# Optimization experiments

Measured on AMD Instinct MI355X. Metric: run time of the kernel, lower is better.

The kernel has to match this reference:

```python
import jax, jax.numpy as jnp
import numpy as np
import math

B, S, H = 2, 2048, 2048
NH, HD = 16, 128
THETA = 10000.0
NEG = -1e9


def make_rope_tables(seq_len, head_dim, theta):
    inv_freq = 1.0 / (theta ** (np.arange(0, head_dim, 2, dtype=np.float32) / head_dim))
    pos = np.arange(seq_len, dtype=np.float32)
    freqs = np.outer(pos, inv_freq)                    # (S, HD/2)
    emb = np.concatenate([freqs, freqs], axis=-1)      # (S, HD)
    return jnp.asarray(np.cos(emb)), jnp.asarray(np.sin(emb))


def setup_inputs() -> dict:
    key = jax.random.key(0)
    k1, k2, k3 = jax.random.split(key, 3)
    hidden_states = jax.random.normal(k1, (B, S, H), dtype=jnp.float32)
    rope_cos, rope_sin = make_rope_tables(S, HD, THETA)
    # additive causal mask [1,1,S,S]
    causal = jnp.tril(jnp.ones((S, S), dtype=bool))
    attention_mask = jnp.where(causal, 0.0, NEG).astype(jnp.float32)[None, None]
    w_qkv = jax.random.normal(k2, (3 * H, H), dtype=jnp.float32) * (1.0 / math.sqrt(H))
    w_o = jax.random.normal(k3, (H, H), dtype=jnp.float32) * (1.0 / math.sqrt(H))
    return {"hidden_states": hidden_states, "rope_cos": rope_cos, "rope_sin": rope_sin,
            "attention_mask": attention_mask, "w_qkv": w_qkv, "w_o": w_o}


def apply_rope(x, cos, sin):
    # x: (B, NH, S, HD); cos/sin: (S, HD)
    half = x.shape[-1] // 2
    x1, x2 = x[..., :half], x[..., half:]
    x_rot = jnp.concatenate([-x2, x1], axis=-1)
    return x * cos[None, None] + x_rot * sin[None, None]


def reference(hidden_states, rope_cos, rope_sin, attention_mask, w_qkv, w_o):
    b, s, h = hidden_states.shape
    qkv = hidden_states @ w_qkv.T                      # (B, S, 3H)
    qkv = qkv.reshape(b, s, 3, NH, HD).transpose(2, 0, 3, 1, 4)  # (3, B, NH, S, HD)
    q, k, v = qkv[0], qkv[1], qkv[2]
    q = apply_rope(q, rope_cos, rope_sin)
    k = apply_rope(k, rope_cos, rope_sin)
    scale = 1.0 / math.sqrt(HD)
    scores = jnp.einsum('bhqd,bhkd->bhqk', q, k) * scale + attention_mask
    probs = jax.nn.softmax(scores.astype(jnp.float32), axis=-1).astype(q.dtype)
    out = jnp.einsum('bhqk,bhkd->bhqd', probs, v)      # (B, NH, S, HD)
    out = out.transpose(0, 2, 1, 3).reshape(b, s, h)
    return out @ w_o.T
```

## Files before the change

### kernel.cpp

```cpp
#include <hip/hip_runtime.h>
#include <stdint.h>

typedef unsigned int u32;
typedef unsigned short u16;

typedef __bf16 bf16x8 __attribute__((ext_vector_type(8)));
typedef float f32x4 __attribute__((ext_vector_type(4)));

struct alignas(16) V16 { u32 a, b, c, d; };

__device__ __forceinline__ u16 f2bf(float x) {
    u32 u = __float_as_uint(x);
    u += 0x7FFFu + ((u >> 16) & 1u);
    return (u16)(u >> 16);
}
__device__ __forceinline__ float bf2f(u16 h) {
    return __uint_as_float(((u32)h) << 16);
}

__device__ __forceinline__ bf16x8 ld_frag(const u16* p) {
    return __builtin_bit_cast(bf16x8, *(const V16*)p);
}

__device__ __forceinline__ void async_cp16(u16* lds_dst, const u16* g_src) {
    __builtin_amdgcn_global_load_lds(
        (__attribute__((address_space(1))) void*)g_src,
        (__attribute__((address_space(3))) void*)lds_dst, 16, 0, 0);
}

__global__ __launch_bounds__(256) void cast_all_kernel(
    const float* __restrict__ hidden, const float* __restrict__ wqkv,
    const float* __restrict__ wo,
    u16* __restrict__ hA, u16* __restrict__ wqb, u16* __restrict__ wob)
{
    int i = blockIdx.x * 256 + threadIdx.x;
    const float* src; u16* dst; int off;
    if (i < 2097152)      { src = hidden; dst = hA;  off = i; }
    else if (i < 5242880) { src = wqkv;   dst = wqb; off = i - 2097152; }
    else                  { src = wo;     dst = wob; off = i - 5242880; }
    const float* p = src + (size_t)off * 4;
    ushort4 o;
    o.x = f2bf(p[0]); o.y = f2bf(p[1]); o.z = f2bf(p[2]); o.w = f2bf(p[3]);
    *(ushort4*)(dst + (size_t)off * 4) = o;
}

__device__ __forceinline__ void stage_half(
    u16* smem, const u16* __restrict__ Ag, const u16* __restrict__ Bg,
    int K, int isB, int kk, int buf, int th, int w, int rg0, int chl)
{
    const u16* G = isB ? Bg : Ag;
    u16* base = smem + isB * 32768 + buf * 16384 + kk * 8192;
    const int kcol = th * 64 + kk * 32;
#pragma unroll
    for (int i = 0; i < 2; ++i) {
        const int s = i * 8 + w;
        const int rg = s * 16 + rg0;
        async_cp16(base + s * 512, G + (size_t)rg * K + kcol + chl * 8);
    }
}

__global__ __launch_bounds__(512, 2) void gemm256(
    const u16* __restrict__ A, const u16* __restrict__ Bt,
    int M, int N, int K, int mode,
    float* __restrict__ Cout,
    u16* __restrict__ Qb, u16* __restrict__ Kb, u16* __restrict__ Vtb)
{
    extern __shared__ u16 smem[];
    const int t = threadIdx.x;
    const int w = t >> 6, l = t & 63;
    const int lr = l & 15, lk = (l >> 4) * 8;
    const int wm16 = (w >> 2) * 8;
    const int wn16 = (w & 3) * 4;
    const int laneoff = lr * 32 + (lk ^ ((lr & 8) ? 16 : 0));
    const int rg0 = l >> 2;
    const int chl = (l & 3) ^ ((l >> 4) & 2);

    const int flat = blockIdx.y * gridDim.x + blockIdx.x;
    const int xcd = flat & 7, slot = flat >> 3;
    const int cpx = gridDim.x >> 3;
    const int ncol = xcd * cpx + slot % cpx;
    const int mrow = slot / cpx;
    const int m0 = mrow * 256, n0 = ncol * 256;

    const u16* Ag = A + (size_t)m0 * K;
    const u16* Bg = Bt + (size_t)n0 * K;

    f32x4 acc[8][4];
#pragma unroll
    for (int i = 0; i < 8; ++i)
#pragma unroll
        for (int j = 0; j < 4; ++j) acc[i][j] = f32x4{0.f, 0.f, 0.f, 0.f};

    const int NT = K >> 6;

    stage_half(smem, Ag, Bg, K, 0, 0, 0, 0, w, rg0, chl);
    stage_half(smem, Ag, Bg, K, 1, 0, 0, 0, w, rg0, chl);
    stage_half(smem, Ag, Bg, K, 0, 1, 0, 0, w, rg0, chl);
    stage_half(smem, Ag, Bg, K, 1, 1, 0, 0, w, rg0, chl);
    stage_half(smem, Ag, Bg, K, 0, 0, 1, 1, w, rg0, chl);
    stage_half(smem, Ag, Bg, K, 1, 0, 1, 1, w, rg0, chl);
    asm volatile("s_waitcnt vmcnt(8)" ::: "memory");
    __builtin_amdgcn_s_barrier();

    for (int tt = 0; tt < NT; tt += 2) {
#pragma unroll
        for (int sub = 0; sub < 2; ++sub) {
            const int tcur = tt + sub;
            const u16* Abuf = smem + sub * 16384;
            const u16* Bbuf = smem + 32768 + sub * 16384;
            bf16x8 bfr[4];
#pragma unroll
            for (int p = 0; p < 4; ++p) {
                const int kk = p >> 1, mh = p & 1;
                const u16* Ab = Abuf + kk * 8192;
                const u16* Bb = Bbuf + kk * 8192;
                if (mh == 0) {
#pragma unroll
                    for (int ni = 0; ni < 4; ++ni)
                        bfr[ni] = ld_frag(Bb + (wn16 + ni) * 512 + laneoff);
                }
                bf16x8 af[4];
#pragma unroll
                for (int i = 0; i < 4; ++i)
                    af[i] = ld_frag(Ab + (wm16 + mh * 4 + i) * 512 + laneoff);

                if (p == 0 && tcur + 1 < NT)
                    stage_half(smem, Ag, Bg, K, 0, 1, sub ^ 1, tcur + 1, w, rg0, chl);
                if (p == 1 && tcur + 1 < NT)
                    stage_half(smem, Ag, Bg, K, 1, 1, sub ^ 1, tcur + 1, w, rg0, chl);
                if (p == 2 && tcur + 2 < NT)
                    stage_half(smem, Ag, Bg, K, 0, 0, sub, tcur + 2, w, rg0, chl);
                if (p == 3 && tcur + 2 < NT)
                    stage_half(smem, Ag, Bg, K, 1, 0, sub, tcur + 2, w, rg0, chl);

                if (p == 1) {
                    if (tcur < NT - 1) asm volatile("s_waitcnt vmcnt(8)" ::: "memory");
                    else               asm volatile("s_waitcnt vmcnt(0)" ::: "memory");
                }
                if (p == 3) {
                    if (tcur < NT - 2)       asm volatile("s_waitcnt vmcnt(8)" ::: "memory");
                    else if (tcur == NT - 2) asm volatile("s_waitcnt vmcnt(4)" ::: "memory");
                }
                __builtin_amdgcn_s_barrier();
                __builtin_amdgcn_s_setprio(1);
#pragma unroll
                for (int i = 0; i < 4; ++i)
#pragma unroll
                    for (int ni = 0; ni < 4; ++ni)
                        acc[mh * 4 + i][ni] = __builtin_amdgcn_mfma_f32_16x16x32_bf16(
                            af[i], bfr[ni], acc[mh * 4 + i][ni], 0, 0, 0);
                __builtin_amdgcn_s_setprio(0);
                __builtin_amdgcn_s_barrier();
            }
        }
    }

    __syncthreads();
    const int lrow4 = (l >> 4) * 4;
    const int wm0 = (w >> 2) * 128, wn0 = (w & 3) * 64;

    if (mode == 1) {
#pragma unroll
        for (int mi = 0; mi < 8; ++mi)
#pragma unroll
            for (int ni = 0; ni < 4; ++ni)
#pragma unroll
                for (int r = 0; r < 4; ++r) {
                    int gr = m0 + wm0 + mi * 16 + lrow4 + r;
                    int gc = n0 + wn0 + ni * 16 + lr;
                    Cout[(size_t)gr * N + gc] = acc[mi][ni][r];
                }
        return;
    }

    const int which = n0 >> 11;
    const int nh0 = (n0 & 2047) >> 7;
    const int bb = m0 >> 11;
    const int s0 = m0 & 2047;

    if (which < 2) {
#pragma unroll
        for (int mi = 0; mi < 8; ++mi)
#pragma unroll
            for (int ni = 0; ni < 4; ++ni)
#pragma unroll
                for (int r = 0; r < 4; ++r)
                    smem[(wm0 + mi * 16 + lrow4 + r) * 256 + wn0 + ni * 16 + lr] =
                        f2bf(acc[mi][ni][r]);
    } else {
#pragma unroll
        for (int mi = 0; mi < 8; ++mi)
#pragma unroll
            for (int ni = 0; ni < 4; ++ni)
#pragma unroll
                for (int r = 0; r < 4; ++r) {
                    int cr = wn0 + ni * 16 + lr;
                    int cc = wm0 + mi * 16 + lrow4 + r;
                    smem[cr * 256 + (cc ^ ((cr & 7) << 3))] = f2bf(acc[mi][ni][r]);
                }
    }
    __syncthreads();

    if (which < 2) {
        u16* dstb = (which == 0 ? Qb : Kb);
#pragma unroll
        for (int ps = 0; ps < 16; ++ps) {
            int chunk = ps * 512 + t;
            int row = chunk >> 5;
            int ce = (chunk & 31) * 8;
            int head = nh0 + (ce >> 7);
            int d = ce & 127;
            *(V16*)&dstb[((size_t)(bb * 16 + head) * 2048 + s0 + row) * 128 + d] =
                *(const V16*)&smem[row * 256 + ce];
        }
    } else {
#pragma unroll
        for (int ps = 0; ps < 16; ++ps) {
            int chunk = ps * 512 + t;
            int drow = chunk >> 5;
            int se = (chunk & 31) * 8;
            int head = nh0 + (drow >> 7);
            int d = drow & 127;
            *(V16*)&Vtb[((size_t)(bb * 16 + head) * 128 + d) * 2048 + s0 + se] =
                *(const V16*)&smem[drow * 256 + (se ^ ((drow & 7) << 3))];
        }
    }
}

__global__ __launch_bounds__(256) void gemm_bt(
    const u16* __restrict__ A, const u16* __restrict__ Bt,
    int M, int N, int K, int mode,
    float* __restrict__ Cout,
    u16* __restrict__ Qb, u16* __restrict__ Kb, u16* __restrict__ Vtb)
{
    __shared__ u16 smem[17408];
    u16* As = smem;
    u16* Bs = smem + 8192;

    const int t = threadIdx.x;
    const int w = t >> 6, l = t & 63;
    const int lr = l & 15;
    const int lk = (l >> 4) * 8;

    const int flat = blockIdx.y * gridDim.x + blockIdx.x;
    const int xcd = flat & 7, slot = flat >> 3;
    const int cpx = gridDim.x >> 3;
    const int ncol = xcd * cpx + slot % cpx;
    const int mrow = slot / cpx;
    const int m0 = mrow * 128, n0 = ncol * 128;
    const int wm = (w >> 1) * 64, wn = (w & 1) * 64;

    f32x4 acc[4][4];
#pragma unroll
    for (int i = 0; i < 4; ++i)
#pragma unroll
        for (int j = 0; j < 4; ++j) acc[i][j] = f32x4{0.f, 0.f, 0.f, 0.f};

    const u16* Ag = A + (size_t)m0 * K;
    const u16* Bg = Bt + (size_t)n0 * K;
    const int srow = l >> 2;
    const int scol = (l & 3) * 8;

    for (int k0 = 0; k0 < K; k0 += 64) {
#pragma unroll
        for (int g = 0; g < 2; ++g) {
            const int row = w * 32 + g * 16;
#pragma unroll
            for (int c = 0; c < 2; ++c) {
                async_cp16(&As[c * 4096 + row * 32],
                           Ag + (size_t)(row + srow) * K + k0 + c * 32 + scol);
                async_cp16(&Bs[c * 4096 + row * 32],
                           Bg + (size_t)(row + srow) * K + k0 + c * 32 + scol);
            }
        }
        __syncthreads();

#pragma unroll
        for (int c = 0; c < 2; ++c) {
            bf16x8 af[4], bf[4];
#pragma unroll
            for (int i = 0; i < 4; ++i)
                af[i] = ld_frag(&As[c * 4096 + (wm + i * 16 + lr) * 32 + lk]);
#pragma unroll
            for (int j = 0; j < 4; ++j)
                bf[j] = ld_frag(&Bs[c * 4096 + (wn + j * 16 + lr) * 32 + lk]);
#pragma unroll
            for (int i = 0; i < 4; ++i)
#pragma unroll
                for (int j = 0; j < 4; ++j)
                    acc[i][j] = __builtin_amdgcn_mfma_f32_16x16x32_bf16(af[i], bf[j], acc[i][j], 0, 0, 0);
        }
        __syncthreads();
    }

    const int lrow4 = (l >> 4) * 4;
    if (mode == 1) {
#pragma unroll
        for (int i = 0; i < 4; ++i)
#pragma unroll
            for (int j = 0; j < 4; ++j)
#pragma unroll
                for (int r = 0; r < 4; ++r) {
                    int gr = m0 + wm + i * 16 + lrow4 + r;
                    int gc = n0 + wn + j * 16 + lr;
                    Cout[(size_t)gr * N + gc] = acc[i][j][r];
                }
    } else {
        const int which = n0 >> 11;
        const int nh = (n0 & 2047) >> 7;
        const int bb = m0 >> 11;
        const int s0 = m0 & 2047;
        u16* Cs = smem;
        if (which < 2) {
#pragma unroll
            for (int i = 0; i < 4; ++i)
#pragma unroll
                for (int j = 0; j < 4; ++j)
#pragma unroll
                    for (int r = 0; r < 4; ++r)
                        Cs[(wm + i * 16 + lrow4 + r) * 136 + wn + j * 16 + lr] =
                            f2bf(acc[i][j][r]);
        } else {
#pragma unroll
            for (int i = 0; i < 4; ++i)
#pragma unroll
                for (int j = 0; j < 4; ++j)
#pragma unroll
                    for (int r = 0; r < 4; ++r)
                        Cs[(wn + j * 16 + lr) * 136 + wm + i * 16 + lrow4 + r] =
                            f2bf(acc[i][j][r]);
        }
        __syncthreads();
        const int rrow = t >> 4, rcol = (t & 15) * 8;
        if (which < 2) {
            u16* dst = (which == 0 ? Qb : Kb) +
                       ((size_t)(bb * 16 + nh) * 2048 + s0) * 128;
#pragma unroll
            for (int it = 0; it < 8; ++it) {
                int row = it * 16 + rrow;
                *(V16*)&dst[(size_t)row * 128 + rcol] = *(const V16*)&Cs[row * 136 + rcol];
            }
        } else {
            u16* dst = Vtb + (size_t)(bb * 16 + nh) * 128 * 2048 + s0;
#pragma unroll
            for (int it = 0; it < 8; ++it) {
                int d = it * 16 + rrow;
                *(V16*)&dst[(size_t)d * 2048 + rcol] = *(const V16*)&Cs[d * 136 + rcol];
            }
        }
    }
}

__global__ __launch_bounds__(256) void rope_kernel(
    u16* __restrict__ Qb, u16* __restrict__ Kb,
    const float* __restrict__ cosT, const float* __restrict__ sinT, float qscale)
{
    int idx = blockIdx.x * 256 + threadIdx.x;
    int d = (idx & 7) * 8;
    int s = (idx >> 3) & 2047;
    int bh = idx >> 14;
    size_t base = ((size_t)bh * 2048 + s) * 128;
    float c[8], sn[8];
#pragma unroll
    for (int i = 0; i < 8; ++i) {
        c[i]  = cosT[s * 128 + d + i];
        sn[i] = sinT[s * 128 + d + i];
    }
    union U { V16 v; u16 h[8]; };
    U qlo, qhi, klo, khi, a, bq, ak, bk;
    qlo.v = *(const V16*)&Qb[base + d];
    qhi.v = *(const V16*)&Qb[base + d + 64];
    klo.v = *(const V16*)&Kb[base + d];
    khi.v = *(const V16*)&Kb[base + d + 64];
#pragma unroll
    for (int i = 0; i < 8; ++i) {
        float q1 = bf2f(qlo.h[i]), q2 = bf2f(qhi.h[i]);
        a.h[i]  = f2bf((q1 * c[i] - q2 * sn[i]) * qscale);
        bq.h[i] = f2bf((q2 * c[i] + q1 * sn[i]) * qscale);
        float k1 = bf2f(klo.h[i]), k2 = bf2f(khi.h[i]);
        ak.h[i] = f2bf(k1 * c[i] - k2 * sn[i]);
        bk.h[i] = f2bf(k2 * c[i] + k1 * sn[i]);
    }
    *(V16*)&Qb[base + d]      = a.v;
    *(V16*)&Qb[base + d + 64] = bq.v;
    *(V16*)&Kb[base + d]      = ak.v;
    *(V16*)&Kb[base + d + 64] = bk.v;
}

#define PS_LD 72
__global__ __launch_bounds__(256, 2) void flash_attn(
    const u16* __restrict__ Qb, const u16* __restrict__ Kb, const u16* __restrict__ Vtb,
    u16* __restrict__ ctx)
{
    __shared__ u16 Ks[64 * 128];
    __shared__ u16 Vts[128 * 64];
    __shared__ u16 Ps[4 * 16 * PS_LD];

    const int t = threadIdx.x, w = t >> 6, l = t & 63;
    const int lr = l & 15, lk = (l >> 4) * 8, lrow4 = (l >> 4) * 4;
    const int hi = l >> 4;
    const int xw = lr & 7;
    const int bh = blockIdx.x;
    const int pidx = blockIdx.y;
    const int wm = w * 16;

    const u16* Qg = Qb + (size_t)bh * 2048 * 128;
    const u16* Kg = Kb + (size_t)bh * 2048 * 128;
    const u16* Vg = Vtb + (size_t)bh * 128 * 2048;
    u16* Pw = &Ps[w * 16 * PS_LD];

    const int krow_l = l >> 4;
    const int vrow_l = l >> 3;
    const int vchk = ((l & 7) ^ vrow_l) * 8;

    const int b = bh >> 4, nh = bh & 15;

#pragma unroll
    for (int half = 0; half < 2; ++half) {
        const int qt = half ? pidx : 31 - pidx;
        const int q0 = qt * 64;

        bf16x8 qfrag[4];
#pragma unroll
        for (int kc = 0; kc < 4; ++kc)
            qfrag[kc] = ld_frag(&Qg[(size_t)(q0 + wm + lr) * 128 + kc * 32 + lk]);

        f32x4 oacc[8];
#pragma unroll
        for (int jo = 0; jo < 8; ++jo) oacc[jo] = f32x4{0.f, 0.f, 0.f, 0.f};
        float l_part[4] = {0.f, 0.f, 0.f, 0.f};

        const int ktiles = qt + 1;
        for (int kt = 0; kt < ktiles; ++kt) {
            const int c0 = kt * 64;
#pragma unroll
            for (int it = 0; it < 4; ++it) {
                const int krow = it * 4 + krow_l;
                const int kchk = ((l & 15) ^ (krow & 7)) * 8;
                async_cp16(&Ks[w * 2048 + it * 512],
                           Kg + (size_t)(c0 + w * 16 + krow) * 128 + kchk);
            }
#pragma unroll
            for (int it = 0; it < 4; ++it) {
                const int vrow = w * 32 + it * 8 + vrow_l;
                async_cp16(&Vts[w * 2048 + it * 512],
                           Vg + (size_t)vrow * 2048 + c0 + vchk);
            }
            __syncthreads();

            f32x4 pacc[4];
#pragma unroll
            for (int j = 0; j < 4; ++j) pacc[j] = f32x4{0.f, 0.f, 0.f, 0.f};
#pragma unroll
            for (int kc = 0; kc < 4; ++kc) {
                const int kco = ((kc * 4 + hi) ^ xw) * 8;
                bf16x8 bk[4];
#pragma unroll
                for (int j = 0; j < 4; ++j)
                    bk[j] = ld_frag(&Ks[(j * 16 + lr) * 128 + kco]);
#pragma unroll
                for (int j = 0; j < 4; ++j)
                    pacc[j] = __builtin_amdgcn_mfma_f32_16x16x32_bf16(qfrag[kc], bk[j], pacc[j], 0, 0, 0);
            }

            if (kt == qt) {
#pragma unroll
                for (int j = 0; j < 4; ++j) {
                    const int cl = j * 16 + lr;
#pragma unroll
                    for (int r = 0; r < 4; ++r) {
                        float pv = (cl > wm + lrow4 + r) ? 0.f : __expf(pacc[j][r]);
                        pacc[j][r] = pv;
                        l_part[r] += pv;
                    }
                }
            } else {
#pragma unroll
                for (int j = 0; j < 4; ++j)
#pragma unroll
                    for (int r = 0; r < 4; ++r) {
                        float pv = __expf(pacc[j][r]);
                        pacc[j][r] = pv;
                        l_part[r] += pv;
                    }
            }

#pragma unroll
            for (int j = 0; j < 4; ++j)
#pragma unroll
                for (int r = 0; r < 4; ++r)
                    Pw[(lrow4 + r) * PS_LD + j * 16 + lr] = f2bf(pacc[j][r]);

#pragma unroll
            for (int kc = 0; kc < 2; ++kc) {
                bf16x8 ap = ld_frag(&Pw[lr * PS_LD + kc * 32 + lk]);
                const int vco = ((kc * 4 + hi) ^ xw) * 8;
#pragma unroll
                for (int jo = 0; jo < 8; ++jo) {
                    bf16x8 bv = ld_frag(&Vts[(jo * 16 + lr) * 64 + vco]);
                    oacc[jo] = __builtin_amdgcn_mfma_f32_16x16x32_bf16(ap, bv, oacc[jo], 0, 0, 0);
                }
            }
            __syncthreads();
        }

        float linv[4];
#pragma unroll
        for (int r = 0; r < 4; ++r) {
            float s = l_part[r];
#pragma unroll
            for (int dd = 8; dd >= 1; dd >>= 1) s += __shfl_xor(s, dd);
            linv[r] = __builtin_amdgcn_rcpf(s);
        }
#pragma unroll
        for (int jo = 0; jo < 8; ++jo)
#pragma unroll
            for (int r = 0; r < 4; ++r) {
                int srow2 = q0 + wm + lrow4 + r;
                int col = nh * 128 + jo * 16 + lr;
                ctx[((size_t)b * 2048 + srow2) * 2048 + col] = f2bf(oacc[jo][r] * linv[r]);
            }
    }
}

extern "C" void kernel_launch(void* const* d_in, const int* in_sizes, int n_in,
                              void* d_out, int out_size, void* d_ws, size_t ws_size,
                              hipStream_t stream)
{
    (void)in_sizes; (void)n_in; (void)out_size; (void)ws_size;
    const float* hidden = (const float*)d_in[0];
    const float* cosT   = (const float*)d_in[1];
    const float* sinT   = (const float*)d_in[2];
    const float* wqkv   = (const float*)d_in[4];
    const float* wo     = (const float*)d_in[5];
    float* out = (float*)d_out;
    char* ws = (char*)d_ws;

    u16* hA   = (u16*)(ws + 0);
    u16* wqb  = (u16*)(ws + 16777216);
    u16* wob  = (u16*)(ws + 41943040);
    u16* Qb   = (u16*)(ws + 50331648);
    u16* Kb   = (u16*)(ws + 67108864);
    u16* Vtb  = (u16*)(ws + 83886080);
    u16* ctx  = (u16*)(ws + 100663296);

    static bool attr_done = false;
    if (!attr_done) {
        hipFuncSetAttribute((const void*)gemm256,
                            hipFuncAttributeMaxDynamicSharedMemorySize, 131072);
        attr_done = true;
    }

    cast_all_kernel<<<dim3(24576), dim3(256), 0, stream>>>(hidden, wqkv, wo,
                                                           hA, wqb, wob);

    gemm256<<<dim3(24, 16), dim3(512), 131072, stream>>>(hA, wqb, 4096, 6144, 2048, 0,
                                                         nullptr, Qb, Kb, Vtb);
    rope_kernel<<<dim3(2048), dim3(256), 0, stream>>>(Qb, Kb, cosT, sinT,
                                                      0.08838834764831845f);

    flash_attn<<<dim3(32, 16), dim3(256), 0, stream>>>(Qb, Kb, Vtb, ctx);

    gemm_bt<<<dim3(16, 32), dim3(256), 0, stream>>>(ctx, wob, 4096, 2048, 2048, 1,
                                                    out, nullptr, nullptr, nullptr);
}
```

Before: 377.4 us.

## Enlarge flash-attention query tile to 128 rows with two row groups per wave

Each block now handles one 128-row query tile, and each wave computes two 16-row groups against every K/V tile staged in shared memory. Before, each block processed two 64-row tiles in sequence. The change halves K/V global loads and LDS staging per query row and gives more MFMA work per barrier. In exchange, register use roughly doubles for the accumulators. Per-block work is also no longer balanced: the old pairing of tiles qt and 31-qt is replaced by a heavy-first ordering, which can cause tail imbalance.

```diff
diff --git a/kernel.cpp b/kernel.cpp
--- a/kernel.cpp
+++ b/kernel.cpp
@@ -394,120 +394,138 @@
 {
     __shared__ u16 Ks[64 * 128];
     __shared__ u16 Vts[128 * 64];
-    __shared__ u16 Ps[4 * 16 * PS_LD];
+    __shared__ u16 Ps[4 * 32 * PS_LD];
 
     const int t = threadIdx.x, w = t >> 6, l = t & 63;
     const int lr = l & 15, lk = (l >> 4) * 8, lrow4 = (l >> 4) * 4;
     const int hi = l >> 4;
     const int xw = lr & 7;
     const int bh = blockIdx.x;
-    const int pidx = blockIdx.y;
-    const int wm = w * 16;
+    const int y = blockIdx.y;
+    const int qt = (y < 8) ? (15 - y) : (y - 8);
+    const int wm = w * 32;
 
     const u16* Qg = Qb + (size_t)bh * 2048 * 128;
     const u16* Kg = Kb + (size_t)bh * 2048 * 128;
     const u16* Vg = Vtb + (size_t)bh * 128 * 2048;
-    u16* Pw = &Ps[w * 16 * PS_LD];
+    u16* Pw = &Ps[w * 32 * PS_LD];
 
     const int krow_l = l >> 4;
     const int vrow_l = l >> 3;
     const int vchk = ((l & 7) ^ vrow_l) * 8;
 
     const int b = bh >> 4, nh = bh & 15;
-
-#pragma unroll
-    for (int half = 0; half < 2; ++half) {
-        const int qt = half ? pidx : 31 - pidx;
-        const int q0 = qt * 64;
-
-        bf16x8 qfrag[4];
+    const int q0 = qt * 128;
+
+    bf16x8 qfrag[2][4];
+#pragma unroll
+    for (int rg = 0; rg < 2; ++rg)
 #pragma unroll
         for (int kc = 0; kc < 4; ++kc)
-            qfrag[kc] = ld_frag(&Qg[(size_t)(q0 + wm + lr) * 128 + kc * 32 + lk]);
-
-        f32x4 oacc[8];
-#pragma unroll
-        for (int jo = 0; jo < 8; ++jo) oacc[jo] = f32x4{0.f, 0.f, 0.f, 0.f};
-        float l_part[4] = {0.f, 0.f, 0.f, 0.f};
-
-        const int ktiles = qt + 1;
-        for (int kt = 0; kt < ktiles; ++kt) {
-            const int c0 = kt * 64;
-#pragma unroll
-            for (int it = 0; it < 4; ++it) {
-                const int krow = it * 4 + krow_l;
-                const int kchk = ((l & 15) ^ (krow & 7)) * 8;
-                async_cp16(&Ks[w * 2048 + it * 512],
-                           Kg + (size_t)(c0 + w * 16 + krow) * 128 + kchk);
+            qfrag[rg][kc] = ld_frag(&Qg[(size_t)(q0 + wm + rg * 16 + lr) * 128 + kc * 32 + lk]);
+
+    f32x4 oacc[2][8];
+#pragma unroll
+    for (int rg = 0; rg < 2; ++rg)
+#pragma unroll
+        for (int jo = 0; jo < 8; ++jo) oacc[rg][jo] = f32x4{0.f, 0.f, 0.f, 0.f};
+    float l_part[2][4] = {{0.f, 0.f, 0.f, 0.f}, {0.f, 0.f, 0.f, 0.f}};
+
+    const int ktiles = 2 * qt + 2;
+    for (int kt = 0; kt < ktiles; ++kt) {
+        const int c0 = kt * 64;
+#pragma unroll
+        for (int it = 0; it < 4; ++it) {
+            const int krow = it * 4 + krow_l;
+            const int kchk = ((l & 15) ^ (krow & 7)) * 8;
+            async_cp16(&Ks[w * 2048 + it * 512],
+                       Kg + (size_t)(c0 + w * 16 + krow) * 128 + kchk);
+        }
+#pragma unroll
+        for (int it = 0; it < 4; ++it) {
+            const int vrow = w * 32 + it * 8 + vrow_l;
+            async_cp16(&Vts[w * 2048 + it * 512],
+                       Vg + (size_t)vrow * 2048 + c0 + vchk);
+        }
+        __syncthreads();
+
+        f32x4 pacc[2][4];
+#pragma unroll
+        for (int rg = 0; rg < 2; ++rg)
+#pragma unroll
+            for (int j = 0; j < 4; ++j) pacc[rg][j] = f32x4{0.f, 0.f, 0.f, 0.f};
+#pragma unroll
+        for (int kc = 0; kc < 4; ++kc) {
+            const int kco = ((kc * 4 + hi) ^ xw) * 8;
+            bf16x8 bk[4];
+#pragma unroll
+            for (int j = 0; j < 4; ++j)
+                bk[j] = ld_frag(&Ks[(j * 16 + lr) * 128 + kco]);
+#pragma unroll
+            for (int rg = 0; rg < 2; ++rg)
+#pragma unroll
+                for (int j = 0; j < 4; ++j)
+                    pacc[rg][j] = __builtin_amdgcn_mfma_f32_16x16x32_bf16(
+                        qfrag[rg][kc], bk[j], pacc[rg][j], 0, 0, 0);
+        }
+
+        if (kt >= 2 * qt) {
+            const int dshift = (kt - 2 * qt) * 64;
+#pragma unroll
+            for (int rg = 0; rg < 2; ++rg)
+#pragma unroll
+                for (int j = 0; j < 4; ++j) {
+                    const int cl = j * 16 + lr + dshift;
+#pragma unroll
+                    for (int r = 0; r < 4; ++r) {
+                        const int row = wm + rg * 16 + lrow4 + r;
+                        float pv = (cl > row) ? 0.f : __expf(pacc[rg][j][r]);
+                        pacc[rg][j][r] = pv;
+                        l_part[rg][r] += pv;
+                    }
+                }
+        } else {
+#pragma unroll
+            for (int rg = 0; rg < 2; ++rg)
+#pragma unroll
+                for (int j = 0; j < 4; ++j)
+#pragma unroll
+                    for (int r = 0; r < 4; ++r) {
+                        float pv = __expf(pacc[rg][j][r]);
+                        pacc[rg][j][r] = pv;
+                        l_part[rg][r] += pv;
+                    }
+        }
+
+#pragma unroll
+        for (int rg = 0; rg < 2; ++rg)
+#pragma unroll
+            for (int j = 0; j < 4; ++j)
+#pragma unroll
+                for (int r = 0; r < 4; ++r)
+                    Pw[(rg * 16 + lrow4 + r) * PS_LD + j * 16 + lr] = f2bf(pacc[rg][j][r]);
+
+#pragma unroll
+        for (int kc = 0; kc < 2; ++kc) {
+            bf16x8 ap0 = ld_frag(&Pw[lr * PS_LD + kc * 32 + lk]);
+            bf16x8 ap1 = ld_frag(&Pw[(16 + lr) * PS_LD + kc * 32 + lk]);
+            const int vco = ((kc * 4 + hi) ^ xw) * 8;
+#pragma unroll
+            for (int jo = 0; jo < 8; ++jo) {
+                bf16x8 bv = ld_frag(&Vts[(jo * 16 + lr) * 64 + vco]);
+                oacc[0][jo] = __builtin_amdgcn_mfma_f32_16x16x32_bf16(ap0, bv, oacc[0][jo], 0, 0, 0);
+                oacc[1][jo] = __builtin_amdgcn_mfma_f32_16x16x32_bf16(ap1, bv, oacc[1][jo], 0, 0, 0);
             }
-#pragma unroll
-            for (int it = 0; it < 4; ++it) {
-                const int vrow = w * 32 + it * 8 + vrow_l;
-                async_cp16(&Vts[w * 2048 + it * 512],
-                           Vg + (size_t)vrow * 2048 + c0 + vchk);
-            }
-            __syncthreads();
-
-            f32x4 pacc[4];
-#pragma unroll
-            for (int j = 0; j < 4; ++j) pacc[j] = f32x4{0.f, 0.f, 0.f, 0.f};
-#pragma unroll
-            for (int kc = 0; kc < 4; ++kc) {
-                const int kco = ((kc * 4 + hi) ^ xw) * 8;
-                bf16x8 bk[4];
-#pragma unroll
-                for (int j = 0; j < 4; ++j)
-                    bk[j] = ld_frag(&Ks[(j * 16 + lr) * 128 + kco]);
-#pragma unroll
-                for (int j = 0; j < 4; ++j)
-                    pacc[j] = __builtin_amdgcn_mfma_f32_16x16x32_bf16(qfrag[kc], bk[j], pacc[j], 0, 0, 0);
-            }
-
-            if (kt == qt) {
-#pragma unroll
-                for (int j = 0; j < 4; ++j) {
-                    const int cl = j * 16 + lr;
-#pragma unroll
-                    for (int r = 0; r < 4; ++r) {
-                        float pv = (cl > wm + lrow4 + r) ? 0.f : __expf(pacc[j][r]);
-                        pacc[j][r] = pv;
-                        l_part[r] += pv;
-                    }
-                }
-            } else {
-#pragma unroll
-                for (int j = 0; j < 4; ++j)
-#pragma unroll
-                    for (int r = 0; r < 4; ++r) {
-                        float pv = __expf(pacc[j][r]);
-                        pacc[j][r] = pv;
-                        l_part[r] += pv;
-                    }
-            }
-
-#pragma unroll
-            for (int j = 0; j < 4; ++j)
-#pragma unroll
-                for (int r = 0; r < 4; ++r)
-                    Pw[(lrow4 + r) * PS_LD + j * 16 + lr] = f2bf(pacc[j][r]);
-
-#pragma unroll
-            for (int kc = 0; kc < 2; ++kc) {
-                bf16x8 ap = ld_frag(&Pw[lr * PS_LD + kc * 32 + lk]);
-                const int vco = ((kc * 4 + hi) ^ xw) * 8;
-#pragma unroll
-                for (int jo = 0; jo < 8; ++jo) {
-                    bf16x8 bv = ld_frag(&Vts[(jo * 16 + lr) * 64 + vco]);
-                    oacc[jo] = __builtin_amdgcn_mfma_f32_16x16x32_bf16(ap, bv, oacc[jo], 0, 0, 0);
-                }
-            }
-            __syncthreads();
-        }
-
+        }
+        __syncthreads();
+    }
+
+#pragma unroll
+    for (int rg = 0; rg < 2; ++rg) {
         float linv[4];
 #pragma unroll
         for (int r = 0; r < 4; ++r) {
-            float s = l_part[r];
+            float s = l_part[rg][r];
 #pragma unroll
             for (int dd = 8; dd >= 1; dd >>= 1) s += __shfl_xor(s, dd);
             linv[r] = __builtin_amdgcn_rcpf(s);
@@ -516,9 +534,9 @@
         for (int jo = 0; jo < 8; ++jo)
 #pragma unroll
             for (int r = 0; r < 4; ++r) {
-                int srow2 = q0 + wm + lrow4 + r;
+                int srow2 = q0 + wm + rg * 16 + lrow4 + r;
                 int col = nh * 128 + jo * 16 + lr;
-                ctx[((size_t)b * 2048 + srow2) * 2048 + col] = f2bf(oacc[jo][r] * linv[r]);
+                ctx[((size_t)b * 2048 + srow2) * 2048 + col] = f2bf(oacc[rg][jo][r] * linv[r]);
             }
     }
 }
```

Measured after the change: 389.0 us. 3.1% more time.
